# Performance work log

Measured on AMD Instinct MI355X. Metric: run time of the kernel, lower is better.

Reference implementation:

```python
import jax, jax.numpy as jnp
import numpy as np

N_NODES = 100000
N_EDGES = 3200000


def gcn_conv(x, edge_index, W, b, n_nodes):
    # PyG GCNConv: x' = D^{-1/2} (A + I) D^{-1/2} (x W) + b
    h = x @ W  # [N, C_out]
    loop = jnp.arange(n_nodes, dtype=edge_index.dtype)
    src = jnp.concatenate([edge_index[0], loop])  # source nodes j
    dst = jnp.concatenate([edge_index[1], loop])  # target nodes i (aggregation)
    deg = jax.ops.segment_sum(jnp.ones_like(dst, h.dtype), dst, num_segments=n_nodes)
    dinv = jnp.where(deg > 0, jax.lax.rsqrt(deg), 0.0)
    norm = dinv[src] * dinv[dst]  # [E+N]
    msg = h[src] * norm[:, None]  # gather + scale
    out = jax.ops.segment_sum(msg, dst, num_segments=n_nodes)  # scatter-add
    return out + b


def setup_inputs() -> dict:
    key = jax.random.key(0)
    ks = jax.random.split(key, 6)
    x = jax.random.normal(ks[0], (N_NODES, 1), dtype=jnp.float32)
    edge_index = jax.random.randint(ks[1], (2, N_EDGES), 0, N_NODES, dtype=jnp.int64)
    W1 = jax.random.normal(ks[2], (1, 16), dtype=jnp.float32) * (1.0 / np.sqrt(1))
    b1 = jnp.zeros((16,), dtype=jnp.float32)
    W2 = jax.random.normal(ks[3], (16, 16), dtype=jnp.float32) * (1.0 / np.sqrt(16))
    b2 = jnp.zeros((16,), dtype=jnp.float32)
    Wl = jax.random.normal(ks[4], (16, 1), dtype=jnp.float32) * (1.0 / np.sqrt(16))
    bl = jnp.zeros((1,), dtype=jnp.float32)
    return {"x": x, "edge_index": edge_index, "W1": W1, "b1": b1,
            "W2": W2, "b2": b2, "Wl": Wl, "bl": bl}


def reference(x, edge_index, W1, b1, W2, b2, Wl, bl):
    n = x.shape[0]
    h = gcn_conv(x, edge_index, W1, b1, n)
    h = jax.nn.relu(h)
    # F.dropout(training=self.training): identity in eval mode
    h = gcn_conv(h, edge_index, W2, b2, n)
    return h @ Wl + bl  # [N, 1]
```

## Files before the change

kernel.cpp:

```cpp
#include <hip/hip_runtime.h>

#define N_NODES  100000
#define N_EDGES  3200000
#define NB       7
#define BSH      14
#define BN       16384
#define PBLK     512
#define PTHR     512
#define PSLICE   6272
#define CAP_SB   1152
#define SA       32
#define GA       (NB * SA)
#define ATHR     1024
#define PPB      (PBLK / SA)
#define RTHR     512


__global__ __launch_bounds__(PTHR) void k_part(const int* __restrict__ src,
        const int* __restrict__ dstp, unsigned* __restrict__ cnt,
        unsigned* __restrict__ pedge) {
    __shared__ unsigned curs[NB];
    const int tid = threadIdx.x, lane = tid & 63;
    if (tid < NB) curs[tid] = 0;
    __syncthreads();
    const int e0 = blockIdx.x * PSLICE;
    const int qbeg = e0 >> 2;
    int qend = (e0 + PSLICE) >> 2;
    const int qmax = N_EDGES >> 2;
    if (qend > qmax) qend = qmax;
    const uint4* s4 = (const uint4*)src;
    const uint4* d4 = (const uint4*)dstp;
    unsigned* myped = pedge + (size_t)blockIdx.x * NB * CAP_SB;

    for (int q = qbeg + tid; q < qend; q += PTHR) {
        const uint4 sv = s4[q], dv = d4[q];
        const unsigned ss[4] = { sv.x, sv.y, sv.z, sv.w };
        const unsigned dd[4] = { dv.x, dv.y, dv.z, dv.w };
        #pragma unroll
        for (int k = 0; k < 4; ++k) {
            const unsigned b = dd[k] >> BSH;
            const unsigned w = ss[k] | ((dd[k] & (BN - 1u)) << 17);
            #pragma unroll
            for (unsigned bb = 0; bb < NB; ++bb) {
                const unsigned long long m = __ballot(b == bb);
                if (m) {
                    const int ldr = __ffsll((long long)m) - 1;
                    unsigned base = 0;
                    if (lane == ldr)
                        base = atomicAdd(&curs[bb], (unsigned)__popcll(m));
                    base = __shfl(base, ldr, 64);
                    if (b == bb) {
                        const unsigned pos =
                            (unsigned)__popcll(m & ((1ull << lane) - 1ull));
                        const unsigned slot = base + pos;
                        if (slot < CAP_SB) myped[bb * CAP_SB + slot] = w;
                    }
                }
            }
        }
    }
    __syncthreads();
    if (tid < NB) {
        unsigned c = curs[tid];
        cnt[blockIdx.x * NB + tid] = c < CAP_SB ? c : CAP_SB;
    }
}

__global__ __launch_bounds__(ATHR) void k_degacc(const unsigned* __restrict__ pedge,
        const unsigned* __restrict__ cnt, unsigned short* __restrict__ p16) {
    __shared__ unsigned facc[BN];
    const int tid = threadIdx.x;
    const int bu = blockIdx.x / SA, sub = blockIdx.x % SA;
    for (int i = tid; i < BN; i += ATHR) facc[i] = 0u;
    __syncthreads();
    #pragma unroll
    for (int r = 0; r < PPB; ++r) {
        const int pb = sub * PPB + r;
        const unsigned n = cnt[pb * NB + bu];
        const unsigned* reg = pedge + ((size_t)pb * NB + bu) * CAP_SB;
        for (unsigned j = tid; j < n; j += ATHR)
            atomicAdd(&facc[reg[j] >> 17], 1u);
    }
    __syncthreads();
    unsigned short* po = p16 + (size_t)blockIdx.x * BN;
    for (int i = tid; i < BN; i += ATHR) po[i] = (unsigned short)facc[i];
}

__global__ __launch_bounds__(RTHR) void k_red1(const float* __restrict__ x,
        const unsigned short* __restrict__ p16,
        float* __restrict__ dinv, float* __restrict__ xs) {
    const int g = blockIdx.x * RTHR + threadIdx.x;
    if (g >= N_NODES) return;
    const int bu = g >> BSH, l = g & (BN - 1);
    const unsigned short* pp = p16 + (size_t)(bu * SA) * BN + l;
    unsigned run = 0;
    #pragma unroll
    for (int s = 0; s < SA; ++s) run += pp[(size_t)s * BN];
    const float di = rsqrtf((float)run + 1.f);
    dinv[g] = di;
    xs[g] = x[g] * di;
}

__global__ __launch_bounds__(ATHR) void k_acc(const unsigned* __restrict__ pedge,
        const unsigned* __restrict__ cnt, const float* __restrict__ vals,
        float* __restrict__ partials) {
    __shared__ float facc[BN];
    const int tid = threadIdx.x;
    const int bu = blockIdx.x / SA, sub = blockIdx.x % SA;
    for (int i = tid; i < BN; i += ATHR) facc[i] = 0.f;
    __syncthreads();
    #pragma unroll
    for (int r = 0; r < PPB; ++r) {
        const int pb = sub * PPB + r;
        const unsigned n = cnt[pb * NB + bu];
        const unsigned* reg = pedge + ((size_t)pb * NB + bu) * CAP_SB;
        for (unsigned j = tid; j < n; j += ATHR) {
            const unsigned w = reg[j];
            atomicAdd(&facc[w >> 17], vals[w & 0x1FFFFu]);
        }
    }
    __syncthreads();
    float* po = partials + (size_t)blockIdx.x * BN;
    for (int i = tid; i < BN; i += ATHR) po[i] = facc[i];
}

__device__ __forceinline__ float sum_partials(const float* __restrict__ partials,
                                              int g) {
    const int bu = g >> BSH, l = g & (BN - 1);
    const float* pp = partials + (size_t)(bu * SA) * BN + l;
    float s = 0.f;
    #pragma unroll
    for (int k = 0; k < SA; ++k) s += pp[(size_t)k * BN];
    return s;
}

__global__ __launch_bounds__(RTHR) void k_red2(const float* __restrict__ x,
        const float* __restrict__ partials, const float* __restrict__ dinv,
        const float* __restrict__ W1, const float* __restrict__ b1,
        const float* __restrict__ W2, const float* __restrict__ Wl,
        float* __restrict__ us, float* __restrict__ uself) {
    const int g = blockIdx.x * RTHR + threadIdx.x;
    if (g >= N_NODES) return;
    const float sum = sum_partials(partials, g);
    const float di = dinv[g];
    const float s1 = di * sum + x[g] * di * di;
    float u = 0.f;
    #pragma unroll
    for (int c = 0; c < 16; ++c) {
        float vcc = 0.f;
        #pragma unroll
        for (int k = 0; k < 16; ++k) vcc += W2[c * 16 + k] * Wl[k];
        u += fmaxf(W1[c] * s1 + b1[c], 0.f) * vcc;
    }
    us[g] = u * di;
    uself[g] = u * di * di;
}

__global__ __launch_bounds__(RTHR) void k_red3(const float* __restrict__ partials,
        const float* __restrict__ dinv, const float* __restrict__ uself,
        const float* __restrict__ W2, const float* __restrict__ b2,
        const float* __restrict__ Wl, const float* __restrict__ bl,
        float* __restrict__ out) {
    const int g = blockIdx.x * RTHR + threadIdx.x;
    if (g >= N_NODES) return;
    const float sum = sum_partials(partials, g);
    float vcb = bl[0];
    #pragma unroll
    for (int c = 0; c < 16; ++c) {
        float vcc = 0.f;
        #pragma unroll
        for (int k = 0; k < 16; ++k) vcc += W2[c * 16 + k] * Wl[k];
        vcb += b2[c] * vcc;
    }
    out[g] = dinv[g] * sum + uself[g] + vcb;
}

extern "C" void kernel_launch(void* const* d_in, const int* in_sizes, int n_in,
                              void* d_out, int out_size, void* d_ws, size_t ws_size,
                              hipStream_t stream) {
    const float* x  = (const float*)d_in[0];
    const int*   ei = (const int*)d_in[1];
    const float* W1 = (const float*)d_in[2];
    const float* b1 = (const float*)d_in[3];
    const float* W2 = (const float*)d_in[4];
    const float* b2 = (const float*)d_in[5];
    const float* Wl = (const float*)d_in[6];
    const float* bl = (const float*)d_in[7];
    float* out = (float*)d_out;

    const int* src  = ei;
    const int* dstp = ei + N_EDGES;

    unsigned* cnt         = (unsigned*)d_ws;
    unsigned* pedge       = cnt + 4096;
    unsigned short* p16   = (unsigned short*)(pedge + (size_t)PBLK * NB * CAP_SB);
    float*    partials    = (float*)(p16 + (size_t)GA * BN);
    float*    dinv        = partials + (size_t)GA * BN;
    float*    xs          = dinv + N_NODES;
    float*    us          = xs + N_NODES;
    float*    uself       = us + N_NODES;

    const int red_blocks = (N_NODES + RTHR - 1) / RTHR;

    k_part<<<PBLK, PTHR, 0, stream>>>(src, dstp, cnt, pedge);
    k_degacc<<<GA, ATHR, 0, stream>>>(pedge, cnt, p16);
    k_red1<<<red_blocks, RTHR, 0, stream>>>(x, p16, dinv, xs);
    k_acc<<<GA, ATHR, 0, stream>>>(pedge, cnt, xs, partials);
    k_red2<<<red_blocks, RTHR, 0, stream>>>(x, partials, dinv, W1, b1, W2, Wl, us, uself);
    k_acc<<<GA, ATHR, 0, stream>>>(pedge, cnt, us, partials);
    k_red3<<<red_blocks, RTHR, 0, stream>>>(partials, dinv, uself, W2, b2, Wl, bl, out);
}
```

Baseline: 187.1 us.

## Stage partitioned edges in LDS and append to contiguous per-bucket global lists

The partition kernel now buffers a tile of 8192 edges in shared memory, computes per-wave bucket offsets with register counters and a wave-level scan, and reserves space in a global per-bucket cursor with one atomic per bucket per block. Each bucket's edges are then written as contiguous runs into one large per-bucket array. The accumulate kernels can stride over a single dense list instead of 16 fixed-capacity sub-slices. This is meant to remove scattered small writes, per-ballot shared atomics and the padding/capacity truncation of the old layout. It adds a memset of the cursor and makes edge order nondeterministic across blocks, which can change float summation order.

```diff
diff --git a/kernel.cpp b/kernel.cpp
--- a/kernel.cpp
+++ b/kernel.cpp
@@ -5,82 +5,120 @@
 #define NB       7
 #define BSH      14
 #define BN       16384
-#define PBLK     512
-#define PTHR     512
-#define PSLICE   6272
-#define CAP_SB   1152
+#define PTHR     1024
+#define NW       16
+#define PTILE    8192
+#define NTILES   ((N_EDGES + PTILE - 1) / PTILE)
+#define CAP_B    600000
 #define SA       32
 #define GA       (NB * SA)
 #define ATHR     1024
-#define PPB      (PBLK / SA)
 #define RTHR     512
 
 
 __global__ __launch_bounds__(PTHR) void k_part(const int* __restrict__ src,
-        const int* __restrict__ dstp, unsigned* __restrict__ cnt,
+        const int* __restrict__ dstp, unsigned* __restrict__ cursor,
         unsigned* __restrict__ pedge) {
-    __shared__ unsigned curs[NB];
-    const int tid = threadIdx.x, lane = tid & 63;
-    if (tid < NB) curs[tid] = 0;
-    __syncthreads();
-    const int e0 = blockIdx.x * PSLICE;
-    const int qbeg = e0 >> 2;
-    int qend = (e0 + PSLICE) >> 2;
-    const int qmax = N_EDGES >> 2;
-    if (qend > qmax) qend = qmax;
+    __shared__ unsigned stage[PTILE];
+    __shared__ unsigned wcnt[NB * NW];
+    __shared__ unsigned woff[NB * NW];
+    __shared__ unsigned bstart[NB + 1];
+    __shared__ unsigned gbase[NB];
+    const int tid = threadIdx.x, wave = tid >> 6, lane = tid & 63;
+    const int qbeg = (blockIdx.x * PTILE) >> 2;
+    int qend = qbeg + (PTILE >> 2);
+    if (qend > (N_EDGES >> 2)) qend = N_EDGES >> 2;
+
     const uint4* s4 = (const uint4*)src;
     const uint4* d4 = (const uint4*)dstp;
-    unsigned* myped = pedge + (size_t)blockIdx.x * NB * CAP_SB;
-
-    for (int q = qbeg + tid; q < qend; q += PTHR) {
-        const uint4 sv = s4[q], dv = d4[q];
+    unsigned pk[8], pos[8];
+    int bk[8];
+    unsigned rc0=0,rc1=0,rc2=0,rc3=0,rc4=0,rc5=0,rc6=0;
+
+    #pragma unroll
+    for (int k = 0; k < 2; ++k) {
+        const int q = qbeg + k * PTHR + tid;
+        const bool v = q < qend;
+        uint4 sv = {0,0,0,0}, dv = {0,0,0,0};
+        if (v) { sv = s4[q]; dv = d4[q]; }
         const unsigned ss[4] = { sv.x, sv.y, sv.z, sv.w };
         const unsigned dd[4] = { dv.x, dv.y, dv.z, dv.w };
         #pragma unroll
-        for (int k = 0; k < 4; ++k) {
-            const unsigned b = dd[k] >> BSH;
-            const unsigned w = ss[k] | ((dd[k] & (BN - 1u)) << 17);
+        for (int j = 0; j < 4; ++j) {
+            const int i = k * 4 + j;
+            const unsigned b = v ? (dd[j] >> BSH) : 0xFFu;
+            bk[i] = v ? (int)b : -1;
+            pk[i] = ss[j] | ((dd[j] & (BN - 1u)) << 17);
+            unsigned p = 0;
             #pragma unroll
             for (unsigned bb = 0; bb < NB; ++bb) {
                 const unsigned long long m = __ballot(b == bb);
-                if (m) {
-                    const int ldr = __ffsll((long long)m) - 1;
-                    unsigned base = 0;
-                    if (lane == ldr)
-                        base = atomicAdd(&curs[bb], (unsigned)__popcll(m));
-                    base = __shfl(base, ldr, 64);
-                    if (b == bb) {
-                        const unsigned pos =
-                            (unsigned)__popcll(m & ((1ull << lane) - 1ull));
-                        const unsigned slot = base + pos;
-                        if (slot < CAP_SB) myped[bb * CAP_SB + slot] = w;
-                    }
-                }
+                const unsigned tot = (unsigned)__popcll(m);
+                const unsigned mb  = (unsigned)__popcll(m & ((1ull << lane) - 1ull));
+                unsigned rcv = bb==0?rc0:bb==1?rc1:bb==2?rc2:bb==3?rc3:bb==4?rc4:bb==5?rc5:rc6;
+                if (b == bb) p = rcv + mb;
+                rcv += tot;
+                if (bb==0) rc0=rcv; else if (bb==1) rc1=rcv; else if (bb==2) rc2=rcv;
+                else if (bb==3) rc3=rcv; else if (bb==4) rc4=rcv; else if (bb==5) rc5=rcv;
+                else rc6=rcv;
             }
+            pos[i] = p;
         }
     }
-    __syncthreads();
-    if (tid < NB) {
-        unsigned c = curs[tid];
-        cnt[blockIdx.x * NB + tid] = c < CAP_SB ? c : CAP_SB;
+    if (lane == 0) wcnt[0 * NW + wave] = rc0;
+    if (lane == 1) wcnt[1 * NW + wave] = rc1;
+    if (lane == 2) wcnt[2 * NW + wave] = rc2;
+    if (lane == 3) wcnt[3 * NW + wave] = rc3;
+    if (lane == 4) wcnt[4 * NW + wave] = rc4;
+    if (lane == 5) wcnt[5 * NW + wave] = rc5;
+    if (lane == 6) wcnt[6 * NW + wave] = rc6;
+    __syncthreads();
+
+    if (wave == 0) {
+        const int i0 = lane * 2, i1 = i0 + 1;
+        unsigned a0 = (i0 < NB * NW) ? wcnt[i0] : 0u;
+        unsigned a1 = (i1 < NB * NW) ? wcnt[i1] : 0u;
+        unsigned ps = a0 + a1;
+        #pragma unroll
+        for (int d = 1; d < 64; d <<= 1) {
+            unsigned o = __shfl_up(ps, d, 64);
+            if (lane >= d) ps += o;
+        }
+        const unsigned excl = ps - (a0 + a1);
+        if (i0 < NB * NW) woff[i0] = excl;
+        if (i1 < NB * NW) woff[i1] = excl + a0;
+        if (lane == 63) bstart[NB] = ps;
+    }
+    __syncthreads();
+    if (tid < NB) bstart[tid] = woff[tid * NW];
+    __syncthreads();
+    if (tid < NB) gbase[tid] = atomicAdd(&cursor[tid], bstart[tid + 1] - bstart[tid]);
+
+    #pragma unroll
+    for (int i = 0; i < 8; ++i)
+        if (bk[i] >= 0) stage[woff[bk[i] * NW + wave] + pos[i]] = pk[i];
+    __syncthreads();
+
+    for (int b = 0; b < NB; ++b) {
+        const unsigned s0 = bstart[b];
+        const unsigned nb2 = bstart[b + 1] - s0;
+        const unsigned g0 = gbase[b];
+        unsigned* dc = pedge + (size_t)b * CAP_B + g0;
+        for (unsigned j = tid; j < nb2; j += PTHR) dc[j] = stage[s0 + j];
     }
 }
 
 __global__ __launch_bounds__(ATHR) void k_degacc(const unsigned* __restrict__ pedge,
-        const unsigned* __restrict__ cnt, unsigned short* __restrict__ p16) {
+        const unsigned* __restrict__ cursor, unsigned short* __restrict__ p16) {
     __shared__ unsigned facc[BN];
     const int tid = threadIdx.x;
     const int bu = blockIdx.x / SA, sub = blockIdx.x % SA;
     for (int i = tid; i < BN; i += ATHR) facc[i] = 0u;
     __syncthreads();
-    #pragma unroll
-    for (int r = 0; r < PPB; ++r) {
-        const int pb = sub * PPB + r;
-        const unsigned n = cnt[pb * NB + bu];
-        const unsigned* reg = pedge + ((size_t)pb * NB + bu) * CAP_SB;
-        for (unsigned j = tid; j < n; j += ATHR)
-            atomicAdd(&facc[reg[j] >> 17], 1u);
-    }
+    const unsigned n = cursor[bu];
+    const unsigned* reg = pedge + (size_t)bu * CAP_B;
+    for (unsigned j = (unsigned)(sub * ATHR + tid); j < n; j += SA * ATHR)
+        atomicAdd(&facc[reg[j] >> 17], 1u);
     __syncthreads();
     unsigned short* po = p16 + (size_t)blockIdx.x * BN;
     for (int i = tid; i < BN; i += ATHR) po[i] = (unsigned short)facc[i];
@@ -102,22 +140,18 @@
 }
 
 __global__ __launch_bounds__(ATHR) void k_acc(const unsigned* __restrict__ pedge,
-        const unsigned* __restrict__ cnt, const float* __restrict__ vals,
+        const unsigned* __restrict__ cursor, const float* __restrict__ vals,
         float* __restrict__ partials) {
     __shared__ float facc[BN];
     const int tid = threadIdx.x;
     const int bu = blockIdx.x / SA, sub = blockIdx.x % SA;
     for (int i = tid; i < BN; i += ATHR) facc[i] = 0.f;
     __syncthreads();
-    #pragma unroll
-    for (int r = 0; r < PPB; ++r) {
-        const int pb = sub * PPB + r;
-        const unsigned n = cnt[pb * NB + bu];
-        const unsigned* reg = pedge + ((size_t)pb * NB + bu) * CAP_SB;
-        for (unsigned j = tid; j < n; j += ATHR) {
-            const unsigned w = reg[j];
-            atomicAdd(&facc[w >> 17], vals[w & 0x1FFFFu]);
-        }
+    const unsigned n = cursor[bu];
+    const unsigned* reg = pedge + (size_t)bu * CAP_B;
+    for (unsigned j = (unsigned)(sub * ATHR + tid); j < n; j += SA * ATHR) {
+        const unsigned w = reg[j];
+        atomicAdd(&facc[w >> 17], vals[w & 0x1FFFFu]);
     }
     __syncthreads();
     float* po = partials + (size_t)blockIdx.x * BN;
@@ -191,22 +225,24 @@
     const int* src  = ei;
     const int* dstp = ei + N_EDGES;
 
-    unsigned* cnt         = (unsigned*)d_ws;
-    unsigned* pedge       = cnt + 4096;
-    unsigned short* p16   = (unsigned short*)(pedge + (size_t)PBLK * NB * CAP_SB);
+    unsigned* cursor      = (unsigned*)d_ws;
+    unsigned* pedge       = cursor + 256;
+    unsigned short* p16   = (unsigned short*)(pedge + (size_t)NB * CAP_B);
     float*    partials    = (float*)(p16 + (size_t)GA * BN);
     float*    dinv        = partials + (size_t)GA * BN;
     float*    xs          = dinv + N_NODES;
     float*    us          = xs + N_NODES;
     float*    uself       = us + N_NODES;
 
+    hipMemsetAsync(d_ws, 0, 64, stream);
+
     const int red_blocks = (N_NODES + RTHR - 1) / RTHR;
 
-    k_part<<<PBLK, PTHR, 0, stream>>>(src, dstp, cnt, pedge);
-    k_degacc<<<GA, ATHR, 0, stream>>>(pedge, cnt, p16);
+    k_part<<<NTILES, PTHR, 0, stream>>>(src, dstp, cursor, pedge);
+    k_degacc<<<GA, ATHR, 0, stream>>>(pedge, cursor, p16);
     k_red1<<<red_blocks, RTHR, 0, stream>>>(x, p16, dinv, xs);
-    k_acc<<<GA, ATHR, 0, stream>>>(pedge, cnt, xs, partials);
+    k_acc<<<GA, ATHR, 0, stream>>>(pedge, cursor, xs, partials);
     k_red2<<<red_blocks, RTHR, 0, stream>>>(x, partials, dinv, W1, b1, W2, Wl, us, uself);
-    k_acc<<<GA, ATHR, 0, stream>>>(pedge, cnt, us, partials);
+    k_acc<<<GA, ATHR, 0, stream>>>(pedge, cursor, us, partials);
     k_red3<<<red_blocks, RTHR, 0, stream>>>(partials, dinv, uself, W2, b2, Wl, bl, out);
 }
```

After: 181.4 us. 1.03x faster.
